# Optimization experiments

Measured on AMD Instinct MI355X. Metric: run time of the kernel, lower is better.

## Reference

```python
import jax, jax.numpy as jnp
import numpy as np

K = 3
PAD = 1
KP = K * K


def setup_inputs() -> dict:
    key = jax.random.key(0)
    k1, k2, k3, k4 = jax.random.split(key, 4)
    B, C, O, H, W = 8, 64, 64, 128, 128
    x = jax.random.normal(k1, (B, C, H, W), dtype=jnp.float32)
    offset = jax.random.normal(k2, (B, 2 * KP, H, W), dtype=jnp.float32)
    weight = jax.random.normal(k3, (O, C, K, K), dtype=jnp.float32) * 0.05
    bias = jax.random.normal(k4, (O,), dtype=jnp.float32) * 0.05
    return {"x": x, "offset": offset, "weight": weight, "bias": bias}


def _deform_conv(x, offset, weight, bias):
    B, C, H, W = x.shape
    O = weight.shape[0]
    x_pad = jnp.pad(x, ((0, 0), (0, 0), (PAD, PAD), (PAD, PAD)))
    Hp, Wp = H + 2 * PAD, W + 2 * PAD
    dt = x.dtype

    # kernel-point grid, row-major (yy, xx) as in torch meshgrid 'ij'
    r = K // 2
    rng = jnp.arange(-r, r + 1, dtype=dt)
    ky = jnp.repeat(rng, K)          # [KP]
    kx = jnp.tile(rng, K)            # [KP]

    base_y = jnp.arange(H, dtype=dt) + PAD
    base_x = jnp.arange(W, dtype=dt) + PAD

    off = offset.reshape(B, KP, 2, H, W)
    # sample coords in padded-image space; grid_sample align_corners=True
    # normalization cancels exactly, so sample at (cy, cx) directly.
    cy = base_y[None, None, :, None] + ky[None, :, None, None] + off[:, :, 0]  # [B,KP,H,W]
    cx = base_x[None, None, None, :] + kx[None, :, None, None] + off[:, :, 1]

    y0 = jnp.floor(cy)
    x0 = jnp.floor(cx)
    wy1 = cy - y0
    wx1 = cx - x0
    wy0 = 1.0 - wy1
    wx0 = 1.0 - wx1

    flat = x_pad.reshape(B, C, Hp * Wp)

    def gather(yi, xi):
        # zeros padding: out-of-bounds corner pixels contribute 0
        valid = ((yi >= 0) & (yi <= Hp - 1) & (xi >= 0) & (xi <= Wp - 1)).astype(dt)
        yc = jnp.clip(yi, 0, Hp - 1).astype(jnp.int32)
        xc = jnp.clip(xi, 0, Wp - 1).astype(jnp.int32)
        idx = (yc * Wp + xc).reshape(B, 1, KP * H * W)
        g = jnp.take_along_axis(flat, jnp.broadcast_to(idx, (B, C, KP * H * W)), axis=2)
        g = g.reshape(B, C, KP, H, W)
        return g * valid[:, None]  # broadcast valid [B,1,KP,H,W]

    sampled = (wy0 * wx0)[:, None] * gather(y0, x0) \
            + (wy0 * wx1)[:, None] * gather(y0, x0 + 1) \
            + (wy1 * wx0)[:, None] * gather(y0 + 1, x0) \
            + (wy1 * wx1)[:, None] * gather(y0 + 1, x0 + 1)  # [B,C,KP,H,W]

    w3 = weight.reshape(O, C, KP)
    out = jnp.einsum('bcphw,ocp->bohw', sampled, w3) + bias[None, :, None, None]
    return out


def reference(x, offset, weight, bias):
    return _deform_conv(x, offset, weight, bias)
```

## Files before the change

kernel.cpp:

```cpp
#include <hip/hip_runtime.h>
#include <hip/hip_bf16.h>

#define BB 8
#define CC 64
#define OO 64
#define HH 128
#define WW 128
#define HP 130
#define WP 130
#define KP 9

typedef __attribute__((ext_vector_type(8))) _Float16 f16x8;
typedef __attribute__((ext_vector_type(2))) _Float16 h2;
typedef __attribute__((ext_vector_type(4))) float f32x4;
typedef __attribute__((ext_vector_type(4))) unsigned u32x4;

#define ROWB 16640u

static __device__ __forceinline__ unsigned short f2h(float f) {
  _Float16 h = (_Float16)f;
  return __builtin_bit_cast(unsigned short, h);
}
static __device__ __forceinline__ h2 asH2(unsigned u) {
  return __builtin_bit_cast(h2, u);
}
static __device__ __forceinline__ unsigned asU32(h2 v) {
  return __builtin_bit_cast(unsigned, v);
}

__global__ __launch_bounds__(256) void k_xpose(const float* __restrict__ x,
                                               const float* __restrict__ wsrc,
                                               unsigned short* __restrict__ xt,
                                               unsigned short* __restrict__ wf) {
  __shared__ unsigned short tile[128][66];
  int wg0 = blockIdx.x;
  int t = threadIdx.x;
  if (wg0 < 144) {
    int flat = wg0 * 256 + t;
    int j = flat & 7;
    int lane = (flat >> 3) & 63;
    int nf = (flat >> 9) & 3;
    int ks = (flat >> 11) & 1;
    int p = flat >> 12;
    int c = ks * 32 + ((lane >> 4) * 8) + j;
    int o = nf * 16 + (lane & 15);
    wf[flat] = f2h(wsrc[(size_t)(o * CC + c) * KP + p]);
  }
  int wg = (wg0 & 7) * 128 + (wg0 >> 3);
  int h = wg & 127, b = wg >> 7;
  int w = t & 127, chalf = t >> 7;
  const float* xp = x + ((size_t)(b * CC) * HH + h) * WW;
#pragma unroll 4
  for (int c2 = 0; c2 < 32; ++c2) {
    int c = c2 * 2 + chalf;
    float v = xp[(size_t)c * HH * WW + w];
    tile[w][c] = f2h(v);
  }
  __syncthreads();
  int c = t & 63, w2 = t >> 6;
  unsigned short* xtb = xt + (size_t)b * HP * WP * CC;
#pragma unroll 4
  for (int w4 = 0; w4 < 32; ++w4) {
    int ww = w4 * 4 + w2;
    xtb[((size_t)(h + 1) * WP + (ww + 1)) * CC + c] = tile[ww][c];
  }
  if (t < 128) {
    int xx = (t >= 64) ? (WP - 1) : 0;
    xtb[((size_t)(h + 1) * WP + xx) * CC + (t & 63)] = 0;
  }
  if (h == 0) {
    for (int i = t; i < 2 * WP * CC; i += 256) {
      int top = (i < WP * CC);
      int rem = top ? i : i - WP * CC;
      size_t y = top ? 0 : (HP - 1);
      xtb[y * WP * CC + rem] = 0;
    }
  }
}

__global__ __launch_bounds__(256) void k_deform_main(const float* __restrict__ offset,
                                                     const float* __restrict__ bias,
                                                     const unsigned short* __restrict__ xt,
                                                     const unsigned short* __restrict__ wf,
                                                     float* __restrict__ out) {
  __shared__ __align__(16) char lds[20992];
  int wg0 = blockIdx.x;
  int wgs = (wg0 & 7) * 256 + (wg0 >> 3);
  int tile = wgs & 1, h = (wgs >> 1) & 127, b = wgs >> 8;
  int w0 = tile * 64;
  int t = threadIdx.x, wave = t >> 6, lane = t & 63;

  char* S0 = lds;
  uint2* cw = reinterpret_cast<uint2*>(lds + 16384) + wave * 144;

#pragma unroll
  for (int it = 0; it < 3; ++it) {
    int pair = it * 64 + lane;
    if (pair < 144) {
      int p = pair >> 4, pxl = pair & 15;
      int px = wave * 16 + pxl;
      int w = w0 + px;
      const float* offp = offset + (((size_t)b * 18 + 2 * p) * HH + h) * WW + w;
      float offy = offp[0];
      float offx = offp[HH * WW];
      float cy = (float)(h + p / 3) + offy;
      float cx = (float)(w + p % 3) + offx;
      float y0f = floorf(cy), x0f = floorf(cx);
      float wy1 = cy - y0f, wx1 = cx - x0f;
      int iy0 = (int)y0f, ix0 = (int)x0f;
      int iy0c = min(max(iy0, 0), HP - 1);
      int iy1c = min(max(iy0 + 1, 0), HP - 1);
      int ix0c = min(max(ix0, 0), WP - 1);
      int ix1c = min(max(ix0 + 1, 0), WP - 1);
      unsigned w0p = (unsigned)((iy0c * WP + ix0c) * (CC * 2));
      if (ix1c != ix0c) w0p |= (1u << 30);
      if (iy1c != iy0c) w0p |= (1u << 31);
      unsigned hv;
      asm("v_cvt_pkrtz_f16_f32 %0, %1, %2" : "=v"(hv) : "v"(wy1), "v"(wx1));
      uint2 ce;
      ce.x = w0p;
      ce.y = hv;
      cw[pair] = ce;
    }
  }

  f32x4 acc[4];
#pragma unroll
  for (int m = 0; m < 4; ++m) acc[m] = (f32x4){0.f, 0.f, 0.f, 0.f};

  const char* xb = (const char*)(xt + (size_t)b * HP * WP * CC);
  int c8 = lane & 7, pg = lane >> 3;
  unsigned cb = (unsigned)c8 * 16;
  unsigned swz = cb ^ ((unsigned)pg << 4);
  const uint2* cwl = cw + pg;

#define GLOADX(dst, voff) \
  asm volatile("global_load_dwordx4 %0, %1, %2" \
               : "=v"(dst) : "v"(voff), "s"(xb) : "memory")
#define GLOADW(dst, voff) \
  asm volatile("global_load_dwordx4 %0, %1, %2" \
               : "=v"(dst) : "v"(voff), "s"(wf) : "memory")

  auto LOADC = [&](int p, uint2* eo) {
#pragma unroll
    for (int it = 0; it < 2; ++it) eo[it] = cwl[p * 16 + it * 8];
  };
  auto ISSUE = [&](const uint2* ei, u32x4* go) {
#pragma unroll
    for (int it = 0; it < 2; ++it) {
      unsigned w0p = ei[it].x;
      unsigned a00 = (w0p & 0x003FFFFFu) + cb;
      unsigned dx = ((w0p >> 30) & 1u) << 7;
      unsigned dy = (w0p & 0x80000000u) ? ROWB : 0u;
      unsigned a01 = a00 + dx, a10 = a00 + dy, a11 = a10 + dx;
      GLOADX(go[it * 4 + 0], a00);
      GLOADX(go[it * 4 + 1], a01);
      GLOADX(go[it * 4 + 2], a10);
      GLOADX(go[it * 4 + 3], a11);
    }
  };
  auto BUILD = [&](const uint2* ei, const u32x4* gi, char* Sc) {
    char* swave = Sc + wave * 2048 + pg * 128;
#pragma unroll
    for (int it = 0; it < 2; ++it) {
      h2 wyx = asH2(ei[it].y);
      _Float16 wy = wyx.x, wx = wyx.y;
      _Float16 w11 = wy * wx;
      _Float16 w01 = wx - w11;
      _Float16 w10 = wy - w11;
      _Float16 w00 = (_Float16)1.0f - wx - w10;
      h2 W00 = {w00, w00}, W01 = {w01, w01}, W10 = {w10, w10}, W11 = {w11, w11};
      u32x4 q00 = gi[it * 4 + 0], q01 = gi[it * 4 + 1];
      u32x4 q10 = gi[it * 4 + 2], q11 = gi[it * 4 + 3];
      u32x4 pk;
#pragma unroll
      for (int k = 0; k < 4; ++k) {
        h2 s = W00 * asH2(q00[k]) + W01 * asH2(q01[k])
             + W10 * asH2(q10[k]) + W11 * asH2(q11[k]);
        pk[k] = asU32(s);
      }
      *reinterpret_cast<u32x4*>(swave + it * 1024 + swz) = pk;
    }
  };
  auto MFMA = [&](const char* Sc, f16x8 b0, f16x8 b1) {
    int l15 = lane & 15, kc = (lane >> 4) * 16, sw = (lane & 7) << 4;
#pragma unroll
    for (int m = 0; m < 4; ++m) {
      int rb = (m * 16 + l15) * 128;
      f16x8 a0 = *reinterpret_cast<const f16x8*>(Sc + rb + (kc ^ sw));
      f16x8 a1 = *reinterpret_cast<const f16x8*>(Sc + rb + ((64 + kc) ^ sw));
      acc[m] = __builtin_amdgcn_mfma_f32_16x16x32_f16(a0, b0, acc[m], 0, 0, 0);
      acc[m] = __builtin_amdgcn_mfma_f32_16x16x32_f16(a1, b1, acc[m], 0, 0, 0);
    }
  };

  uint2 e[2];
  u32x4 g[8];
  f16x8 bvA0, bvA1, bvB0, bvB1;
  LOADC(0, e);
  ISSUE(e, g);
  {
    unsigned wfo = (unsigned)((0 * 8 + wave) * 1024 + lane * 16);
    GLOADW(bvA0, wfo);
    GLOADW(bvA1, wfo + 4096);
  }

#pragma unroll
  for (int p = 0; p < 9; ++p) {
    char* Sc = S0 + (p & 1) * 8192;
    asm volatile("s_waitcnt vmcnt(0)" ::: "memory");
    __builtin_amdgcn_sched_barrier(0);
    BUILD(e, g, Sc);
    if (p < 8) {
      LOADC(p + 1, e);
      ISSUE(e, g);
      unsigned wfo = (unsigned)(((p + 1) * 8 + wave) * 1024 + lane * 16);
      if (p & 1) { GLOADW(bvA0, wfo); GLOADW(bvA1, wfo + 4096); }
      else       { GLOADW(bvB0, wfo); GLOADW(bvB1, wfo + 4096); }
    }
    asm volatile("s_waitcnt lgkmcnt(0)" ::: "memory");
    __builtin_amdgcn_s_barrier();
    if (p & 1) MFMA(Sc, bvB0, bvB1);
    else       MFMA(Sc, bvA0, bvA1);
  }
#undef GLOADX
#undef GLOADW

  __syncthreads();
  float* S2 = reinterpret_cast<float*>(lds);
  int l15 = lane & 15;
#pragma unroll
  for (int m = 0; m < 4; ++m) {
#pragma unroll
    for (int i2 = 0; i2 < 4; ++i2) {
      int px = m * 16 + ((lane >> 4) * 4) + i2;
      int o = wave * 16 + l15;
      S2[px * 65 + o] = acc[m][i2];
    }
  }
  __syncthreads();
  {
    int px = t & 63, o2 = t >> 6;
    float* op = out + (((size_t)b * OO) * HH + h) * WW + w0 + px;
#pragma unroll
    for (int o4 = 0; o4 < 16; ++o4) {
      int o = o4 * 4 + o2;
      op[(size_t)o * HH * WW] = S2[px * 65 + o] + bias[o];
    }
  }
}

extern "C" void kernel_launch(void* const* d_in, const int* in_sizes, int n_in,
                              void* d_out, int out_size, void* d_ws, size_t ws_size,
                              hipStream_t stream) {
  const float* x = (const float*)d_in[0];
  const float* offset = (const float*)d_in[1];
  const float* weight = (const float*)d_in[2];
  const float* bias = (const float*)d_in[3];
  float* out = (float*)d_out;

  unsigned short* xt = (unsigned short*)d_ws;
  unsigned short* wf = (unsigned short*)((char*)d_ws + 17305600);

  k_xpose<<<BB * HH, 256, 0, stream>>>(x, weight, xt, wf);
  k_deform_main<<<BB * HH * 2, 256, 0, stream>>>(offset, bias, xt, wf, out);
}
```

Baseline: 46.41 us.

## Stage weights in LDS and make each wave own its pixel tile

The main loop changes from "each wave computes 16 output channels across all 64 pixels" to "each wave computes all 64 output channels for its own 16 sampled pixels". Each wave now reads only the A fragment it built itself, so the per-tap workgroup barrier and the double-buffered shared sample tile go away. Weights for the kernel points are copied into LDS in two batches (5 then 4 taps), each batch framed by syncthreads, and are read from LDS instead of per-wave global loads. This raises LDS use to about 53 KB per block, which may cut occupancy. It also adds two bulk weight-copy phases per block.

```diff
diff --git a/kernel.cpp b/kernel.cpp
--- a/kernel.cpp
+++ b/kernel.cpp
@@ -83,15 +83,16 @@
                                                      const unsigned short* __restrict__ xt,
                                                      const unsigned short* __restrict__ wf,
                                                      float* __restrict__ out) {
-  __shared__ __align__(16) char lds[20992];
+  __shared__ __align__(16) char lds[53760];
   int wg0 = blockIdx.x;
   int wgs = (wg0 & 7) * 256 + (wg0 >> 3);
   int tile = wgs & 1, h = (wgs >> 1) & 127, b = wgs >> 8;
   int w0 = tile * 64;
   int t = threadIdx.x, wave = t >> 6, lane = t & 63;
 
-  char* S0 = lds;
-  uint2* cw = reinterpret_cast<uint2*>(lds + 16384) + wave * 144;
+  uint2* cw = reinterpret_cast<uint2*>(lds + 8192) + wave * 144;
+  char* Sw = lds + wave * 2048;
+  char* wlds = lds + 12800;
 
 #pragma unroll
   for (int it = 0; it < 3; ++it) {
@@ -137,9 +138,6 @@
 #define GLOADX(dst, voff) \
   asm volatile("global_load_dwordx4 %0, %1, %2" \
                : "=v"(dst) : "v"(voff), "s"(xb) : "memory")
-#define GLOADW(dst, voff) \
-  asm volatile("global_load_dwordx4 %0, %1, %2" \
-               : "=v"(dst) : "v"(voff), "s"(wf) : "memory")
 
   auto LOADC = [&](int p, uint2* eo) {
 #pragma unroll
@@ -159,8 +157,8 @@
       GLOADX(go[it * 4 + 3], a11);
     }
   };
-  auto BUILD = [&](const uint2* ei, const u32x4* gi, char* Sc) {
-    char* swave = Sc + wave * 2048 + pg * 128;
+  auto BUILD = [&](const uint2* ei, const u32x4* gi) {
+    char* swave = Sw + pg * 128;
 #pragma unroll
     for (int it = 0; it < 2; ++it) {
       h2 wyx = asH2(ei[it].y);
@@ -182,60 +180,75 @@
       *reinterpret_cast<u32x4*>(swave + it * 1024 + swz) = pk;
     }
   };
-  auto MFMA = [&](const char* Sc, f16x8 b0, f16x8 b1) {
+  auto MFMA = [&](int prel) {
     int l15 = lane & 15, kc = (lane >> 4) * 16, sw = (lane & 7) << 4;
-#pragma unroll
-    for (int m = 0; m < 4; ++m) {
-      int rb = (m * 16 + l15) * 128;
-      f16x8 a0 = *reinterpret_cast<const f16x8*>(Sc + rb + (kc ^ sw));
-      f16x8 a1 = *reinterpret_cast<const f16x8*>(Sc + rb + ((64 + kc) ^ sw));
-      acc[m] = __builtin_amdgcn_mfma_f32_16x16x32_f16(a0, b0, acc[m], 0, 0, 0);
-      acc[m] = __builtin_amdgcn_mfma_f32_16x16x32_f16(a1, b1, acc[m], 0, 0, 0);
+    const char* Swr = Sw + l15 * 128;
+    f16x8 a0 = *reinterpret_cast<const f16x8*>(Swr + (kc ^ sw));
+    f16x8 a1 = *reinterpret_cast<const f16x8*>(Swr + ((64 + kc) ^ sw));
+    const char* wp = wlds + prel * 8192 + lane * 16;
+#pragma unroll
+    for (int nf = 0; nf < 4; ++nf) {
+      f16x8 b0 = *reinterpret_cast<const f16x8*>(wp + nf * 1024);
+      f16x8 b1 = *reinterpret_cast<const f16x8*>(wp + 4096 + nf * 1024);
+      acc[nf] = __builtin_amdgcn_mfma_f32_16x16x32_f16(a0, b0, acc[nf], 0, 0, 0);
+      acc[nf] = __builtin_amdgcn_mfma_f32_16x16x32_f16(a1, b1, acc[nf], 0, 0, 0);
     }
   };
 
   uint2 e[2];
   u32x4 g[8];
-  f16x8 bvA0, bvA1, bvB0, bvB1;
   LOADC(0, e);
   ISSUE(e, g);
   {
-    unsigned wfo = (unsigned)((0 * 8 + wave) * 1024 + lane * 16);
-    GLOADW(bvA0, wfo);
-    GLOADW(bvA1, wfo + 4096);
-  }
-
-#pragma unroll
-  for (int p = 0; p < 9; ++p) {
-    char* Sc = S0 + (p & 1) * 8192;
+    const u32x4* srcw = reinterpret_cast<const u32x4*>(wf);
+    u32x4* dstw = reinterpret_cast<u32x4*>(wlds);
+#pragma unroll
+    for (int i = 0; i < 10; ++i) dstw[i * 256 + t] = srcw[i * 256 + t];
+  }
+  __syncthreads();
+
+#pragma unroll
+  for (int p = 0; p < 5; ++p) {
     asm volatile("s_waitcnt vmcnt(0)" ::: "memory");
     __builtin_amdgcn_sched_barrier(0);
-    BUILD(e, g, Sc);
+    BUILD(e, g);
+    LOADC(p + 1, e);
+    ISSUE(e, g);
+    MFMA(p);
+  }
+
+  __syncthreads();
+  {
+    const u32x4* srcw = reinterpret_cast<const u32x4*>(wf) + 2560;
+    u32x4* dstw = reinterpret_cast<u32x4*>(wlds);
+#pragma unroll
+    for (int i = 0; i < 8; ++i) dstw[i * 256 + t] = srcw[i * 256 + t];
+  }
+  __syncthreads();
+
+#pragma unroll
+  for (int p = 5; p < 9; ++p) {
+    asm volatile("s_waitcnt vmcnt(0)" ::: "memory");
+    __builtin_amdgcn_sched_barrier(0);
+    BUILD(e, g);
     if (p < 8) {
       LOADC(p + 1, e);
       ISSUE(e, g);
-      unsigned wfo = (unsigned)(((p + 1) * 8 + wave) * 1024 + lane * 16);
-      if (p & 1) { GLOADW(bvA0, wfo); GLOADW(bvA1, wfo + 4096); }
-      else       { GLOADW(bvB0, wfo); GLOADW(bvB1, wfo + 4096); }
-    }
-    asm volatile("s_waitcnt lgkmcnt(0)" ::: "memory");
-    __builtin_amdgcn_s_barrier();
-    if (p & 1) MFMA(Sc, bvB0, bvB1);
-    else       MFMA(Sc, bvA0, bvA1);
+    }
+    MFMA(p - 5);
   }
 #undef GLOADX
-#undef GLOADW
 
   __syncthreads();
   float* S2 = reinterpret_cast<float*>(lds);
   int l15 = lane & 15;
 #pragma unroll
-  for (int m = 0; m < 4; ++m) {
+  for (int nf = 0; nf < 4; ++nf) {
 #pragma unroll
     for (int i2 = 0; i2 < 4; ++i2) {
-      int px = m * 16 + ((lane >> 4) * 4) + i2;
-      int o = wave * 16 + l15;
-      S2[px * 65 + o] = acc[m][i2];
+      int px = wave * 16 + ((lane >> 4) * 4) + i2;
+      int o = nf * 16 + l15;
+      S2[px * 65 + o] = acc[nf][i2];
     }
   }
   __syncthreads();
```

Measured after the change: 48.49 us. 1.04x slower.
